# Performance work log

Hardware: AMD Instinct MI355X
Metric: run time of the kernel (lower is better)

Reference implementation:

```python
import jax, jax.numpy as jnp
import numpy as np

B, T, D = 2, 2048, 512
HEADS, DIM_HEAD, MAX_LAG = 8, 64, 5
INNER = HEADS * DIM_HEAD


def setup_inputs() -> dict:
    key = jax.random.key(0)
    k0, k1, k2, k3, k4 = jax.random.split(key, 5)
    x = jax.random.normal(k0, (B, T, D), dtype=jnp.float32)
    # Linear weights stored as (in, out); torch applies x @ W.T with W (out, in).
    Wq = jax.random.normal(k1, (D, INNER), dtype=jnp.float32) * (1.0 / np.sqrt(D))
    Wk = jax.random.normal(k2, (D, INNER), dtype=jnp.float32) * (1.0 / np.sqrt(D))
    Wv = jax.random.normal(k3, (D, INNER), dtype=jnp.float32) * (1.0 / np.sqrt(D))
    Wo = jax.random.normal(k4, (INNER, D), dtype=jnp.float32) * (1.0 / np.sqrt(INNER))
    bo = jnp.zeros((D,), dtype=jnp.float32)
    # Module's init: lag_weights = log(exp(-lags/(max_lag/3))) = -lags/(max_lag/3)
    lags = jnp.arange(MAX_LAG + 1, dtype=jnp.float32)
    lag_weights = jnp.broadcast_to(-(lags / (MAX_LAG / 3.0)), (HEADS, MAX_LAG + 1)).astype(jnp.float32)
    return {"x": x, "Wq": Wq, "Wk": Wk, "Wv": Wv, "Wo": Wo, "bo": bo, "lag_weights": lag_weights}


def reference(x, Wq, Wk, Wv, Wo, bo, lag_weights):
    b, t, _ = x.shape
    h, dh = HEADS, DIM_HEAD
    scale = dh ** -0.5
    # context defaults to x (self-attention)
    q = (x @ Wq).reshape(b, t, h, dh).transpose(0, 2, 1, 3)  # b h t d
    k = (x @ Wk).reshape(b, t, h, dh).transpose(0, 2, 1, 3)
    v = (x @ Wv).reshape(b, t, h, dh).transpose(0, 2, 1, 3)
    sim = jnp.einsum('bhid,bhjd->bhij', q, k) * scale  # b h t t
    # causal mask: keep j <= i
    causal = jnp.tril(jnp.ones((t, t), dtype=bool))
    neg = -jnp.finfo(sim.dtype).max
    sim = jnp.where(causal[None, None], sim, neg)
    # learned additive time-lag bias: lag_adj[h,i,j] = softmax(lag_weights)[h, clamp(i-j,0,MAX_LAG)]
    ti = jnp.arange(t)
    time_lags = jnp.clip(ti[:, None] - ti[None, :], 0, MAX_LAG)  # t t
    lag_probs = jax.nn.softmax(lag_weights, axis=-1)  # h (L+1)
    lag_adj = lag_probs[:, time_lags]  # h t t
    sim = sim + lag_adj[None]
    attn = jax.nn.softmax(sim, axis=-1)
    out = jnp.einsum('bhij,bhjd->bhid', attn, v)
    out = out.transpose(0, 2, 1, 3).reshape(b, t, h * dh)  # b t inner
    return out @ Wo + bo  # dropout is identity at eval
```

## Files before the change

kernel.cpp:

```cpp
#include <hip/hip_runtime.h>
#include <hip/hip_bf16.h>

#define BB 2
#define TT 2048
#define DD 512
#define HH 8
#define DH 64
#define INNER 512
#define MAXLAG 5

typedef __attribute__((ext_vector_type(8))) short short8;
typedef __attribute__((ext_vector_type(4))) float floatx4;
typedef unsigned short ushort_t;

__device__ inline unsigned short f2bf(float f) {
    unsigned u = __float_as_uint(f);
    unsigned r = (u + 0x7FFFu + ((u >> 16) & 1u)) >> 16;
    return (unsigned short)r;
}
__device__ inline float bf2f(unsigned short u) {
    return __uint_as_float(((unsigned)u) << 16);
}

__device__ __forceinline__ void gload16(ushort_t* lds, const ushort_t* g) {
    __builtin_amdgcn_global_load_lds(
        (const __attribute__((address_space(1))) void*)g,
        (__attribute__((address_space(3))) void*)lds, 16, 0, 0);
}

__global__ __launch_bounds__(256)
void cvt_kernel(const float* __restrict__ x,
                const float* __restrict__ wq, const float* __restrict__ wk,
                const float* __restrict__ wv, const float* __restrict__ wo,
                ushort_t* __restrict__ xb,
                ushort_t* __restrict__ wqkvt, ushort_t* __restrict__ wot)
{
    __shared__ float T[32][33];
    const int bid = blockIdx.x;
    if (bid < 1024) {
        int off = (bid * 256 + threadIdx.x) * 8;
        float4 a = *(const float4*)&x[off];
        float4 b = *(const float4*)&x[off + 4];
        ushort_t t[8];
        t[0] = f2bf(a.x); t[1] = f2bf(a.y); t[2] = f2bf(a.z); t[3] = f2bf(a.w);
        t[4] = f2bf(b.x); t[5] = f2bf(b.y); t[6] = f2bf(b.z); t[7] = f2bf(b.w);
        *(uint4*)&xb[off] = *(const uint4*)t;
        return;
    }
    const int r = bid - 1024;
    const int z = r >> 8;
    const int tile = r & 255;
    const float* s = (z == 0) ? wq : (z == 1) ? wk : (z == 2) ? wv : wo;
    ushort_t*    d = (z < 3) ? (wqkvt + (size_t)z * 512 * 512) : wot;
    const int k0 = (tile & 15) * 32;
    const int n0 = (tile >> 4) * 32;
    {
        const int kk = threadIdx.x >> 3;
        const int n4 = (threadIdx.x & 7) * 4;
        float4 v = *(const float4*)&s[(size_t)(k0 + kk) * 512 + n0 + n4];
        T[kk][n4 + 0] = v.x; T[kk][n4 + 1] = v.y;
        T[kk][n4 + 2] = v.z; T[kk][n4 + 3] = v.w;
    }
    __syncthreads();
    {
        const int nn = threadIdx.x >> 3;
        const int k4 = (threadIdx.x & 7) * 4;
        ushort4 o;
        o.x = f2bf(T[k4 + 0][nn]); o.y = f2bf(T[k4 + 1][nn]);
        o.z = f2bf(T[k4 + 2][nn]); o.w = f2bf(T[k4 + 3][nn]);
        *(ushort4*)&d[(size_t)(n0 + nn) * 512 + k0 + k4] = o;
    }
}

#define QM 128
#define QN 64
#define QKS 64

__global__ __launch_bounds__(256)
void gemm_qkv(const ushort_t* __restrict__ A, const ushort_t* __restrict__ Bw,
              ushort_t* __restrict__ q, ushort_t* __restrict__ k,
              ushort_t* __restrict__ vt)
{
    __shared__ ushort_t As[QM * QKS];
    __shared__ ushort_t Bs[QN * QKS];

    const int tid  = threadIdx.x;
    const int wave = tid >> 6;
    const int lane = tid & 63;
    const int quad = lane >> 4;
    const int l15  = lane & 15;
    const int wr   = wave >> 1;
    const int wc   = wave & 1;
    const int bm   = blockIdx.y * QM;
    const int bn   = blockIdx.x * QN;

    const int ga = wave * 256 + lane;
    const ushort_t* ap0 = &A[(size_t)(bm + ((ga +   0) >> 3)) * DD + ((ga +   0) & 7) * 8];
    const ushort_t* ap1 = &A[(size_t)(bm + ((ga +  64) >> 3)) * DD + ((ga +  64) & 7) * 8];
    const ushort_t* ap2 = &A[(size_t)(bm + ((ga + 128) >> 3)) * DD + ((ga + 128) & 7) * 8];
    const ushort_t* ap3 = &A[(size_t)(bm + ((ga + 192) >> 3)) * DD + ((ga + 192) & 7) * 8];
    const int gb = wave * 128 + lane;
    const ushort_t* bp0 = &Bw[(size_t)(bn + ((gb +  0) >> 3)) * DD + ((gb +  0) & 7) * 8];
    const ushort_t* bp1 = &Bw[(size_t)(bn + ((gb + 64) >> 3)) * DD + ((gb + 64) & 7) * 8];
    ushort_t* lA0 = &As[(size_t)(wave * 256 +   0) * 8];
    ushort_t* lA1 = &As[(size_t)(wave * 256 +  64) * 8];
    ushort_t* lA2 = &As[(size_t)(wave * 256 + 128) * 8];
    ushort_t* lA3 = &As[(size_t)(wave * 256 + 192) * 8];
    ushort_t* lB0 = &Bs[(size_t)(wave * 128 +  0) * 8];
    ushort_t* lB1 = &Bs[(size_t)(wave * 128 + 64) * 8];

    floatx4 acc[4][2];
#pragma unroll
    for (int i = 0; i < 4; ++i)
#pragma unroll
        for (int j = 0; j < 2; ++j) acc[i][j] = (floatx4){0.f, 0.f, 0.f, 0.f};

    for (int k0 = 0; k0 < DD; k0 += QKS) {
        __syncthreads();
        gload16(lA0, ap0 + k0);
        gload16(lA1, ap1 + k0);
        gload16(lA2, ap2 + k0);
        gload16(lA3, ap3 + k0);
        gload16(lB0, bp0 + k0);
        gload16(lB1, bp1 + k0);
        __syncthreads();

#pragma unroll
        for (int kk = 0; kk < 2; ++kk) {
            short8 af[4], bfr[2];
#pragma unroll
            for (int mt = 0; mt < 4; ++mt)
                af[mt] = *(const short8*)
                    &As[(((wr * 64 + mt * 16 + l15) << 3) + (kk << 2) + quad) * 8];
#pragma unroll
            for (int nt = 0; nt < 2; ++nt)
                bfr[nt] = *(const short8*)
                    &Bs[(((wc * 32 + nt * 16 + l15) << 3) + (kk << 2) + quad) * 8];
#pragma unroll
            for (int mt = 0; mt < 4; ++mt)
#pragma unroll
                for (int nt = 0; nt < 2; ++nt)
                    acc[mt][nt] = __builtin_amdgcn_mfma_f32_16x16x32_bf16(
                        af[mt], bfr[nt], acc[mt][nt], 0, 0, 0);
        }
    }

    const int z = bn >> 9;
    if (z == 2) {
#pragma unroll
        for (int mt = 0; mt < 4; ++mt) {
            const int m0 = bm + wr * 64 + mt * 16 + quad * 4;
            const int b  = m0 >> 11;
            const int t0 = m0 & 2047;
#pragma unroll
            for (int nt = 0; nt < 2; ++nt) {
                const int n  = bn + wc * 32 + nt * 16 + l15 - 1024;
                const int h  = n >> 6, dd = n & 63;
                ushort4 o;
                o.x = f2bf(acc[mt][nt][0]); o.y = f2bf(acc[mt][nt][1]);
                o.z = f2bf(acc[mt][nt][2]); o.w = f2bf(acc[mt][nt][3]);
                *(ushort4*)&vt[((size_t)((b * 8 + h) * 64 + dd)) * 2048 + t0] = o;
            }
        }
        return;
    }
    ushort_t* O = (z == 0) ? q : k;
    const int nb = bn - z * 512;
#pragma unroll
    for (int mt = 0; mt < 4; ++mt) {
#pragma unroll
        for (int nt = 0; nt < 2; ++nt) {
            const int n = nb + wc * 32 + nt * 16 + l15;
#pragma unroll
            for (int reg = 0; reg < 4; ++reg) {
                const int m = bm + wr * 64 + mt * 16 + quad * 4 + reg;
                O[(size_t)m * 512 + n] = f2bf(acc[mt][nt][reg]);
            }
        }
    }
}

__global__ __launch_bounds__(256)
void gemm_proj(const ushort_t* __restrict__ A, const ushort_t* __restrict__ Bw,
               float* __restrict__ O, const float* __restrict__ bias)
{
    __shared__ ushort_t As[64 * 64];
    __shared__ ushort_t Bs[64 * 64];

    const int tid  = threadIdx.x;
    const int wave = tid >> 6;
    const int lane = tid & 63;
    const int quad = lane >> 4;
    const int l15  = lane & 15;
    const int wr   = wave >> 1;
    const int wc   = wave & 1;
    const int bm   = blockIdx.y * 64;
    const int bn   = blockIdx.x * 64;

    const int g0 = wave * 128 + lane;
    const ushort_t* ap0 = &A[(size_t)(bm + ((g0 +  0) >> 3)) * INNER + ((g0 +  0) & 7) * 8];
    const ushort_t* ap1 = &A[(size_t)(bm + ((g0 + 64) >> 3)) * INNER + ((g0 + 64) & 7) * 8];
    const ushort_t* bp0 = &Bw[(size_t)(bn + ((g0 +  0) >> 3)) * INNER + ((g0 +  0) & 7) * 8];
    const ushort_t* bp1 = &Bw[(size_t)(bn + ((g0 + 64) >> 3)) * INNER + ((g0 + 64) & 7) * 8];
    ushort_t* lA0 = &As[(size_t)(wave * 128 +  0) * 8];
    ushort_t* lA1 = &As[(size_t)(wave * 128 + 64) * 8];
    ushort_t* lB0 = &Bs[(size_t)(wave * 128 +  0) * 8];
    ushort_t* lB1 = &Bs[(size_t)(wave * 128 + 64) * 8];

    floatx4 acc[2][2];
#pragma unroll
    for (int i = 0; i < 2; ++i)
#pragma unroll
        for (int j = 0; j < 2; ++j) acc[i][j] = (floatx4){0.f, 0.f, 0.f, 0.f};

    for (int k0 = 0; k0 < INNER; k0 += 64) {
        __syncthreads();
        gload16(lA0, ap0 + k0);
        gload16(lA1, ap1 + k0);
        gload16(lB0, bp0 + k0);
        gload16(lB1, bp1 + k0);
        __syncthreads();

#pragma unroll
        for (int kk = 0; kk < 2; ++kk) {
            short8 af[2], bfr[2];
#pragma unroll
            for (int mt = 0; mt < 2; ++mt)
                af[mt] = *(const short8*)
                    &As[(((wr * 32 + mt * 16 + l15) << 3) + (kk << 2) + quad) * 8];
#pragma unroll
            for (int nt = 0; nt < 2; ++nt)
                bfr[nt] = *(const short8*)
                    &Bs[(((wc * 32 + nt * 16 + l15) << 3) + (kk << 2) + quad) * 8];
#pragma unroll
            for (int mt = 0; mt < 2; ++mt)
#pragma unroll
                for (int nt = 0; nt < 2; ++nt)
                    acc[mt][nt] = __builtin_amdgcn_mfma_f32_16x16x32_bf16(
                        af[mt], bfr[nt], acc[mt][nt], 0, 0, 0);
        }
    }

    float bv[2];
#pragma unroll
    for (int nt = 0; nt < 2; ++nt)
        bv[nt] = bias[bn + wc * 32 + nt * 16 + l15];
#pragma unroll
    for (int mt = 0; mt < 2; ++mt) {
#pragma unroll
        for (int nt = 0; nt < 2; ++nt) {
            const int n = bn + wc * 32 + nt * 16 + l15;
#pragma unroll
            for (int reg = 0; reg < 4; ++reg) {
                const int m = bm + wr * 32 + mt * 16 + quad * 4 + reg;
                O[(size_t)m * 512 + n] = acc[mt][nt][reg] + bv[nt];
            }
        }
    }
}

#define PAD 72
#define MFIX 10.0f

__global__ __launch_bounds__(256)
void attn_mfma(const ushort_t* __restrict__ Qg,
               const ushort_t* __restrict__ Kg,
               const ushort_t* __restrict__ Vtg,
               const float* __restrict__ lagw,
               ushort_t* __restrict__ ao)
{
    __shared__ ushort_t Ks[64 * 8 * 8];
    __shared__ ushort_t Vts[64 * 8 * 8];
    __shared__ ushort_t Pl[4][16][PAD];

    const int tid  = threadIdx.x;
    const int wave = tid >> 6;
    const int lane = tid & 63;
    const int quad = lane >> 4;
    const int l15  = lane & 15;

    const int f    = blockIdx.x + 32 * blockIdx.y;
    const int half = f >> 8;
    const int r    = f & 255;
    const int bh   = (half << 3) | (r >> 5);
    const int qt   = half ? (r & 31) : (31 - (r & 31));
    const int b    = bh >> 3;
    const int h    = bh & 7;
    const int i0   = qt * 64;
    const int hi   = qt + 1;

    float lagb[MAXLAG + 1];
    {
        float mx = -1e30f;
#pragma unroll
        for (int l = 0; l <= MAXLAG; ++l) {
            lagb[l] = lagw[h * (MAXLAG + 1) + l];
            mx = fmaxf(mx, lagb[l]);
        }
        float s = 0.f;
#pragma unroll
        for (int l = 0; l <= MAXLAG; ++l) { lagb[l] = __expf(lagb[l] - mx); s += lagb[l]; }
        float inv = 1.f / s;
#pragma unroll
        for (int l = 0; l <= MAXLAG; ++l) lagb[l] = lagb[l] * inv - MFIX;
    }
    const float c1  = 0.125f;
    const float c2f = lagb[MAXLAG];

    short8 qf0, qf1;
    {
        const ushort_t* qbase =
            Qg + ((size_t)(b * TT + i0 + wave * 16 + l15)) * INNER + h * DH;
        qf0 = *(const short8*)(qbase + quad * 8);
        qf1 = *(const short8*)(qbase + 32 + quad * 8);
    }

    floatx4 oacc[4];
    float lsum[4] = {0.f, 0.f, 0.f, 0.f};
#pragma unroll
    for (int cb = 0; cb < 4; ++cb) oacc[cb] = (floatx4){0.f, 0.f, 0.f, 0.f};

    const int ibase = i0 + wave * 16 + quad * 4;

    const int srow = tid >> 3;
    const int sc   = tid & 7;
    const ushort_t* Kp0 = Kg + ((size_t)(b * TT) + srow) * INNER + h * DH + sc * 8;
    const ushort_t* Kp1 = Kp0 + (size_t)32 * INNER;
    const ushort_t* Vp0 = Vtg + ((size_t)(bh * 64 + srow)) * 2048 + sc * 8;
    const ushort_t* Vp1 = Vp0 + (size_t)32 * 2048;
    const int slot = (sc + srow) & 7;
    const int kdst0 = ((srow << 3) + slot) << 3;
    const int kdst1 = (((srow + 32) << 3) + slot) << 3;

    uint4 pk0 = *(const uint4*)Kp0;
    uint4 pk1 = *(const uint4*)Kp1;
    uint4 pv0 = *(const uint4*)Vp0;
    uint4 pv1 = *(const uint4*)Vp1;

    for (int kt = 0; kt < hi; ++kt) {
        __syncthreads();
        *(uint4*)&Ks[kdst0]  = pk0;
        *(uint4*)&Ks[kdst1]  = pk1;
        *(uint4*)&Vts[kdst0] = pv0;
        *(uint4*)&Vts[kdst1] = pv1;
        if (kt + 1 < hi) {
            const size_t koff = (size_t)((kt + 1) * 64) * INNER;
            pk0 = *(const uint4*)(Kp0 + koff);
            pk1 = *(const uint4*)(Kp1 + koff);
            pv0 = *(const uint4*)(Vp0 + (kt + 1) * 64);
            pv1 = *(const uint4*)(Vp1 + (kt + 1) * 64);
        }
        __syncthreads();

        const int j0 = kt * 64;

        floatx4 sacc[4];
#pragma unroll
        for (int cb = 0; cb < 4; ++cb) {
            const int key = cb * 16 + l15;
            short8 kf0 = *(const short8*)&Ks[((key << 3) + ((quad + key) & 7)) << 3];
            short8 kf1 = *(const short8*)&Ks[((key << 3) + ((quad + 4 + key) & 7)) << 3];
            floatx4 zf = (floatx4){0.f, 0.f, 0.f, 0.f};
            zf = __builtin_amdgcn_mfma_f32_16x16x32_bf16(qf0, kf0, zf, 0, 0, 0);
            zf = __builtin_amdgcn_mfma_f32_16x16x32_bf16(qf1, kf1, zf, 0, 0, 0);
            sacc[cb] = zf;
        }

        float p[4][4];
        if (i0 + wave * 16 - (j0 + 63) >= MAXLAG) {
#pragma unroll
            for (int cb = 0; cb < 4; ++cb)
#pragma unroll
                for (int reg = 0; reg < 4; ++reg)
                    p[cb][reg] = __expf(fmaf(sacc[cb][reg], c1, c2f));
        } else {
#pragma unroll
            for (int cb = 0; cb < 4; ++cb) {
                const int j = j0 + cb * 16 + l15;
#pragma unroll
                for (int reg = 0; reg < 4; ++reg) {
                    const int lag = (ibase + reg) - j;
                    float bias = (lag <= 0) ? lagb[0]
                               : (lag == 1) ? lagb[1]
                               : (lag == 2) ? lagb[2]
                               : (lag == 3) ? lagb[3]
                               : (lag == 4) ? lagb[4] : lagb[5];
                    float e = __expf(fmaf(sacc[cb][reg], c1, bias));
                    p[cb][reg] = (lag < 0) ? 0.f : e;
                }
            }
        }
#pragma unroll
        for (int cb = 0; cb < 4; ++cb)
#pragma unroll
            for (int reg = 0; reg < 4; ++reg)
                lsum[reg] += p[cb][reg];

#pragma unroll
        for (int cb = 0; cb < 4; ++cb)
#pragma unroll
            for (int reg = 0; reg < 4; ++reg)
                Pl[wave][quad * 4 + reg][cb * 16 + l15] = f2bf(p[cb][reg]);

        short8 pf0 = *(const short8*)&Pl[wave][l15][quad * 8];
        short8 pf1 = *(const short8*)&Pl[wave][l15][32 + quad * 8];

#pragma unroll
        for (int cb = 0; cb < 4; ++cb) {
            const int dd = cb * 16 + l15;
            short8 vf0 = *(const short8*)&Vts[((dd << 3) + ((quad + dd) & 7)) << 3];
            short8 vf1 = *(const short8*)&Vts[((dd << 3) + ((quad + 4 + dd) & 7)) << 3];
            oacc[cb] = __builtin_amdgcn_mfma_f32_16x16x32_bf16(pf0, vf0, oacc[cb], 0, 0, 0);
            oacc[cb] = __builtin_amdgcn_mfma_f32_16x16x32_bf16(pf1, vf1, oacc[cb], 0, 0, 0);
        }
    }

#pragma unroll
    for (int reg = 0; reg < 4; ++reg) {
        lsum[reg] += __shfl_xor(lsum[reg], 1);
        lsum[reg] += __shfl_xor(lsum[reg], 2);
        lsum[reg] += __shfl_xor(lsum[reg], 4);
        lsum[reg] += __shfl_xor(lsum[reg], 8);
    }

#pragma unroll
    for (int reg = 0; reg < 4; ++reg) {
        const int row = ibase + reg;
        const float inv = 1.f / lsum[reg];
        ushort_t* dst = &ao[((size_t)(b * TT + row)) * INNER + h * DH];
#pragma unroll
        for (int cb = 0; cb < 4; ++cb)
            dst[cb * 16 + l15] = f2bf(oacc[cb][reg] * inv);
    }
}

extern "C" void kernel_launch(void* const* d_in, const int* in_sizes, int n_in,
                              void* d_out, int out_size, void* d_ws, size_t ws_size,
                              hipStream_t stream)
{
    const float* x  = (const float*)d_in[0];
    const float* Wq = (const float*)d_in[1];
    const float* Wk = (const float*)d_in[2];
    const float* Wv = (const float*)d_in[3];
    const float* Wo = (const float*)d_in[4];
    const float* bo = (const float*)d_in[5];
    const float* lw = (const float*)d_in[6];
    float* out = (float*)d_out;

    const size_t SZ  = (size_t)BB * TT * INNER;
    const size_t NWE = (size_t)DD * INNER;
    ushort_t* xb    = (ushort_t*)d_ws;
    ushort_t* wqkvt = xb + SZ;
    ushort_t* wot   = wqkvt + 3 * NWE;
    ushort_t* q     = wot + NWE;
    ushort_t* k     = q + SZ;
    ushort_t* vt    = k + SZ;
    ushort_t* ao    = xb;

    cvt_kernel<<<2048, 256, 0, stream>>>(x, Wq, Wk, Wv, Wo, xb, wqkvt, wot);

    dim3 gQKV(3 * INNER / QN, (BB * TT) / QM);
    gemm_qkv<<<gQKV, 256, 0, stream>>>(xb, wqkvt, q, k, vt);

    dim3 gATT(32, BB * HH);
    attn_mfma<<<gATT, 256, 0, stream>>>(q, k, vt, lw, ao);

    dim3 gPRJ(DD / 64, (BB * TT) / 64);
    gemm_proj<<<gPRJ, 256, 0, stream>>>(ao, wot, out, bo);
}
```

Baseline: 130.1 us.

## Double-buffer LDS tiles with swizzled direct loads in GEMM and attention kernels

The QKV GEMM, output projection GEMM and attention kernel now use two LDS buffers. The next K-tile is issued with gload16 into the idle buffer while MFMAs run on the current one, so each iteration needs one barrier instead of two. The GEMM tiles get an XOR-style column swizzle on both the global source offsets and the LDS reads, to cut bank conflicts. The attention kernel drops its register-staged prefetch for direct global-to-LDS loads and wraps its MFMA blocks in s_setprio. The cost is doubled LDS footprint, which may lower occupancy.

```diff
diff --git a/kernel.cpp b/kernel.cpp
--- a/kernel.cpp
+++ b/kernel.cpp
@@ -81,8 +81,8 @@
               ushort_t* __restrict__ q, ushort_t* __restrict__ k,
               ushort_t* __restrict__ vt)
 {
-    __shared__ ushort_t As[QM * QKS];
-    __shared__ ushort_t Bs[QN * QKS];
+    __shared__ ushort_t As[2][QM * QKS];
+    __shared__ ushort_t Bs[2][QN * QKS];
 
     const int tid  = threadIdx.x;
     const int wave = tid >> 6;
@@ -94,20 +94,32 @@
     const int bm   = blockIdx.y * QM;
     const int bn   = blockIdx.x * QN;
 
-    const int ga = wave * 256 + lane;
-    const ushort_t* ap0 = &A[(size_t)(bm + ((ga +   0) >> 3)) * DD + ((ga +   0) & 7) * 8];
-    const ushort_t* ap1 = &A[(size_t)(bm + ((ga +  64) >> 3)) * DD + ((ga +  64) & 7) * 8];
-    const ushort_t* ap2 = &A[(size_t)(bm + ((ga + 128) >> 3)) * DD + ((ga + 128) & 7) * 8];
-    const ushort_t* ap3 = &A[(size_t)(bm + ((ga + 192) >> 3)) * DD + ((ga + 192) & 7) * 8];
-    const int gb = wave * 128 + lane;
-    const ushort_t* bp0 = &Bw[(size_t)(bn + ((gb +  0) >> 3)) * DD + ((gb +  0) & 7) * 8];
-    const ushort_t* bp1 = &Bw[(size_t)(bn + ((gb + 64) >> 3)) * DD + ((gb + 64) & 7) * 8];
-    ushort_t* lA0 = &As[(size_t)(wave * 256 +   0) * 8];
-    ushort_t* lA1 = &As[(size_t)(wave * 256 +  64) * 8];
-    ushort_t* lA2 = &As[(size_t)(wave * 256 + 128) * 8];
-    ushort_t* lA3 = &As[(size_t)(wave * 256 + 192) * 8];
-    ushort_t* lB0 = &Bs[(size_t)(wave * 128 +  0) * 8];
-    ushort_t* lB1 = &Bs[(size_t)(wave * 128 + 64) * 8];
+    const int lr = lane >> 3;
+    const int lc = lane & 7;
+
+    const ushort_t* ap[4];
+#pragma unroll
+    for (int j = 0; j < 4; ++j) {
+        const int row = wave * 32 + j * 8 + lr;
+        const int c   = (lc - row) & 7;
+        ap[j] = &A[(size_t)(bm + row) * DD + c * 8];
+    }
+    const ushort_t* bp[2];
+#pragma unroll
+    for (int j = 0; j < 2; ++j) {
+        const int row = wave * 16 + j * 8 + lr;
+        const int c   = (lc - row) & 7;
+        bp[j] = &Bw[(size_t)(bn + row) * DD + c * 8];
+    }
+
+    auto stage = [&](int buf, int koff) {
+#pragma unroll
+        for (int j = 0; j < 4; ++j)
+            gload16(&As[buf][(wave * 256 + j * 64) * 8], ap[j] + koff);
+#pragma unroll
+        for (int j = 0; j < 2; ++j)
+            gload16(&Bs[buf][(wave * 128 + j * 64) * 8], bp[j] + koff);
+    };
 
     floatx4 acc[4][2];
 #pragma unroll
@@ -115,27 +127,28 @@
 #pragma unroll
         for (int j = 0; j < 2; ++j) acc[i][j] = (floatx4){0.f, 0.f, 0.f, 0.f};
 
+    stage(0, 0);
+    __syncthreads();
+    int cur = 0;
     for (int k0 = 0; k0 < DD; k0 += QKS) {
-        __syncthreads();
-        gload16(lA0, ap0 + k0);
-        gload16(lA1, ap1 + k0);
-        gload16(lA2, ap2 + k0);
-        gload16(lA3, ap3 + k0);
-        gload16(lB0, bp0 + k0);
-        gload16(lB1, bp1 + k0);
-        __syncthreads();
+        const int nxt = k0 + QKS;
+        if (nxt < DD) stage(cur ^ 1, nxt);
 
 #pragma unroll
         for (int kk = 0; kk < 2; ++kk) {
             short8 af[4], bfr[2];
 #pragma unroll
-            for (int mt = 0; mt < 4; ++mt)
+            for (int mt = 0; mt < 4; ++mt) {
+                const int row = wr * 64 + mt * 16 + l15;
                 af[mt] = *(const short8*)
-                    &As[(((wr * 64 + mt * 16 + l15) << 3) + (kk << 2) + quad) * 8];
-#pragma unroll
-            for (int nt = 0; nt < 2; ++nt)
+                    &As[cur][((row << 3) + ((kk * 4 + quad + row) & 7)) * 8];
+            }
+#pragma unroll
+            for (int nt = 0; nt < 2; ++nt) {
+                const int row = wc * 32 + nt * 16 + l15;
                 bfr[nt] = *(const short8*)
-                    &Bs[(((wc * 32 + nt * 16 + l15) << 3) + (kk << 2) + quad) * 8];
+                    &Bs[cur][((row << 3) + ((kk * 4 + quad + row) & 7)) * 8];
+            }
 #pragma unroll
             for (int mt = 0; mt < 4; ++mt)
 #pragma unroll
@@ -143,6 +156,8 @@
                     acc[mt][nt] = __builtin_amdgcn_mfma_f32_16x16x32_bf16(
                         af[mt], bfr[nt], acc[mt][nt], 0, 0, 0);
         }
+        if (nxt < DD) __syncthreads();
+        cur ^= 1;
     }
 
     const int z = bn >> 9;
@@ -184,8 +199,8 @@
 void gemm_proj(const ushort_t* __restrict__ A, const ushort_t* __restrict__ Bw,
                float* __restrict__ O, const float* __restrict__ bias)
 {
-    __shared__ ushort_t As[64 * 64];
-    __shared__ ushort_t Bs[64 * 64];
+    __shared__ ushort_t As[2][64 * 64];
+    __shared__ ushort_t Bs[2][64 * 64];
 
     const int tid  = threadIdx.x;
     const int wave = tid >> 6;
@@ -197,15 +212,26 @@
     const int bm   = blockIdx.y * 64;
     const int bn   = blockIdx.x * 64;
 
-    const int g0 = wave * 128 + lane;
-    const ushort_t* ap0 = &A[(size_t)(bm + ((g0 +  0) >> 3)) * INNER + ((g0 +  0) & 7) * 8];
-    const ushort_t* ap1 = &A[(size_t)(bm + ((g0 + 64) >> 3)) * INNER + ((g0 + 64) & 7) * 8];
-    const ushort_t* bp0 = &Bw[(size_t)(bn + ((g0 +  0) >> 3)) * INNER + ((g0 +  0) & 7) * 8];
-    const ushort_t* bp1 = &Bw[(size_t)(bn + ((g0 + 64) >> 3)) * INNER + ((g0 + 64) & 7) * 8];
-    ushort_t* lA0 = &As[(size_t)(wave * 128 +  0) * 8];
-    ushort_t* lA1 = &As[(size_t)(wave * 128 + 64) * 8];
-    ushort_t* lB0 = &Bs[(size_t)(wave * 128 +  0) * 8];
-    ushort_t* lB1 = &Bs[(size_t)(wave * 128 + 64) * 8];
+    const int lr = lane >> 3;
+    const int lc = lane & 7;
+
+    const ushort_t* ap[2];
+    const ushort_t* bp[2];
+#pragma unroll
+    for (int j = 0; j < 2; ++j) {
+        const int row = wave * 16 + j * 8 + lr;
+        const int c   = (lc - row) & 7;
+        ap[j] = &A[(size_t)(bm + row) * INNER + c * 8];
+        bp[j] = &Bw[(size_t)(bn + row) * INNER + c * 8];
+    }
+
+    auto stage = [&](int buf, int koff) {
+#pragma unroll
+        for (int j = 0; j < 2; ++j) {
+            gload16(&As[buf][(wave * 128 + j * 64) * 8], ap[j] + koff);
+            gload16(&Bs[buf][(wave * 128 + j * 64) * 8], bp[j] + koff);
+        }
+    };
 
     floatx4 acc[2][2];
 #pragma unroll
@@ -213,25 +239,28 @@
 #pragma unroll
         for (int j = 0; j < 2; ++j) acc[i][j] = (floatx4){0.f, 0.f, 0.f, 0.f};
 
+    stage(0, 0);
+    __syncthreads();
+    int cur = 0;
     for (int k0 = 0; k0 < INNER; k0 += 64) {
-        __syncthreads();
-        gload16(lA0, ap0 + k0);
-        gload16(lA1, ap1 + k0);
-        gload16(lB0, bp0 + k0);
-        gload16(lB1, bp1 + k0);
-        __syncthreads();
+        const int nxt = k0 + 64;
+        if (nxt < INNER) stage(cur ^ 1, nxt);
 
 #pragma unroll
         for (int kk = 0; kk < 2; ++kk) {
             short8 af[2], bfr[2];
 #pragma unroll
-            for (int mt = 0; mt < 2; ++mt)
+            for (int mt = 0; mt < 2; ++mt) {
+                const int row = wr * 32 + mt * 16 + l15;
                 af[mt] = *(const short8*)
-                    &As[(((wr * 32 + mt * 16 + l15) << 3) + (kk << 2) + quad) * 8];
-#pragma unroll
-            for (int nt = 0; nt < 2; ++nt)
+                    &As[cur][((row << 3) + ((kk * 4 + quad + row) & 7)) * 8];
+            }
+#pragma unroll
+            for (int nt = 0; nt < 2; ++nt) {
+                const int row = wc * 32 + nt * 16 + l15;
                 bfr[nt] = *(const short8*)
-                    &Bs[(((wc * 32 + nt * 16 + l15) << 3) + (kk << 2) + quad) * 8];
+                    &Bs[cur][((row << 3) + ((kk * 4 + quad + row) & 7)) * 8];
+            }
 #pragma unroll
             for (int mt = 0; mt < 2; ++mt)
 #pragma unroll
@@ -239,6 +268,8 @@
                     acc[mt][nt] = __builtin_amdgcn_mfma_f32_16x16x32_bf16(
                         af[mt], bfr[nt], acc[mt][nt], 0, 0, 0);
         }
+        if (nxt < INNER) __syncthreads();
+        cur ^= 1;
     }
 
     float bv[2];
@@ -269,8 +300,8 @@
                const float* __restrict__ lagw,
                ushort_t* __restrict__ ao)
 {
-    __shared__ ushort_t Ks[64 * 8 * 8];
-    __shared__ ushort_t Vts[64 * 8 * 8];
+    __shared__ ushort_t Ks[2][64 * 8 * 8];
+    __shared__ ushort_t Vts[2][64 * 8 * 8];
     __shared__ ushort_t Pl[4][16][PAD];
 
     const int tid  = threadIdx.x;
@@ -322,49 +353,50 @@
 
     const int ibase = i0 + wave * 16 + quad * 4;
 
-    const int srow = tid >> 3;
-    const int sc   = tid & 7;
-    const ushort_t* Kp0 = Kg + ((size_t)(b * TT) + srow) * INNER + h * DH + sc * 8;
-    const ushort_t* Kp1 = Kp0 + (size_t)32 * INNER;
-    const ushort_t* Vp0 = Vtg + ((size_t)(bh * 64 + srow)) * 2048 + sc * 8;
-    const ushort_t* Vp1 = Vp0 + (size_t)32 * 2048;
-    const int slot = (sc + srow) & 7;
-    const int kdst0 = ((srow << 3) + slot) << 3;
-    const int kdst1 = (((srow + 32) << 3) + slot) << 3;
-
-    uint4 pk0 = *(const uint4*)Kp0;
-    uint4 pk1 = *(const uint4*)Kp1;
-    uint4 pv0 = *(const uint4*)Vp0;
-    uint4 pv1 = *(const uint4*)Vp1;
+    const int lr = lane >> 3;
+    const int lc = lane & 7;
+    const ushort_t* ksrc[2];
+    const ushort_t* vsrc[2];
+#pragma unroll
+    for (int j = 0; j < 2; ++j) {
+        const int row = wave * 16 + j * 8 + lr;
+        const int c   = (lc - row) & 7;
+        ksrc[j] = Kg + ((size_t)(b * TT) + row) * INNER + h * DH + c * 8;
+        vsrc[j] = Vtg + ((size_t)(bh * 64 + row)) * 2048 + c * 8;
+    }
+
+    auto stage = [&](int buf, int kt) {
+        const size_t ko = (size_t)kt * 64 * INNER;
+        const int    vo = kt * 64;
+#pragma unroll
+        for (int j = 0; j < 2; ++j) {
+            gload16(&Ks[buf][(wave * 128 + j * 64) * 8],  ksrc[j] + ko);
+            gload16(&Vts[buf][(wave * 128 + j * 64) * 8], vsrc[j] + vo);
+        }
+    };
+
+    stage(0, 0);
+    __syncthreads();
+    int cur = 0;
 
     for (int kt = 0; kt < hi; ++kt) {
-        __syncthreads();
-        *(uint4*)&Ks[kdst0]  = pk0;
-        *(uint4*)&Ks[kdst1]  = pk1;
-        *(uint4*)&Vts[kdst0] = pv0;
-        *(uint4*)&Vts[kdst1] = pv1;
-        if (kt + 1 < hi) {
-            const size_t koff = (size_t)((kt + 1) * 64) * INNER;
-            pk0 = *(const uint4*)(Kp0 + koff);
-            pk1 = *(const uint4*)(Kp1 + koff);
-            pv0 = *(const uint4*)(Vp0 + (kt + 1) * 64);
-            pv1 = *(const uint4*)(Vp1 + (kt + 1) * 64);
-        }
-        __syncthreads();
+        if (kt + 1 < hi) stage(cur ^ 1, kt + 1);
 
         const int j0 = kt * 64;
 
         floatx4 sacc[4];
+        __builtin_amdgcn_s_setprio(1);
 #pragma unroll
         for (int cb = 0; cb < 4; ++cb) {
             const int key = cb * 16 + l15;
-            short8 kf0 = *(const short8*)&Ks[((key << 3) + ((quad + key) & 7)) << 3];
-            short8 kf1 = *(const short8*)&Ks[((key << 3) + ((quad + 4 + key) & 7)) << 3];
+            short8 kf0 = *(const short8*)&Ks[cur][((key << 3) + ((quad + key) & 7)) << 3];
+            short8 kf1 = *(const short8*)&Ks[cur][((key << 3) + ((quad + 4 + key) & 7)) << 3];
             floatx4 zf = (floatx4){0.f, 0.f, 0.f, 0.f};
             zf = __builtin_amdgcn_mfma_f32_16x16x32_bf16(qf0, kf0, zf, 0, 0, 0);
             zf = __builtin_amdgcn_mfma_f32_16x16x32_bf16(qf1, kf1, zf, 0, 0, 0);
             sacc[cb] = zf;
         }
+        __builtin_amdgcn_s_setprio(0);
 
         float p[4][4];
         if (i0 + wave * 16 - (j0 + 63) >= MAXLAG) {
@@ -405,14 +437,19 @@
         short8 pf0 = *(const short8*)&Pl[wave][l15][quad * 8];
         short8 pf1 = *(const short8*)&Pl[wave][l15][32 + quad * 8];
 
+        __builtin_amdgcn_s_setprio(1);
 #pragma unroll
         for (int cb = 0; cb < 4; ++cb) {
             const int dd = cb * 16 + l15;
-            short8 vf0 = *(const short8*)&Vts[((dd << 3) + ((quad + dd) & 7)) << 3];
-            short8 vf1 = *(const short8*)&Vts[((dd << 3) + ((quad + 4 + dd) & 7)) << 3];
+            short8 vf0 = *(const short8*)&Vts[cur][((dd << 3) + ((quad + dd) & 7)) << 3];
+            short8 vf1 = *(const short8*)&Vts[cur][((dd << 3) + ((quad + 4 + dd) & 7)) << 3];
             oacc[cb] = __builtin_amdgcn_mfma_f32_16x16x32_bf16(pf0, vf0, oacc[cb], 0, 0, 0);
             oacc[cb] = __builtin_amdgcn_mfma_f32_16x16x32_bf16(pf1, vf1, oacc[cb], 0, 0, 0);
         }
+        __builtin_amdgcn_s_setprio(0);
+
+        if (kt + 1 < hi) __syncthreads();
+        cur ^= 1;
     }
 
 #pragma unroll
```

Measured after the change: 137.0 us. +5.3%, slower.

## Split attention key range into chunks and add a combine kernel

Applied to the files above, without the earlier changes.

Each query tile's causal key range is split into chunks of up to 8 key tiles, processed by separate blocks (1280 total). Each block writes an unnormalized bf16 partial output and a row sum. A new combine kernel sums the partials and normalizes. This shortens the per-block critical path and improves CU load balance, at the cost of an extra launch, extra global traffic, and bf16 rounding of the partials.

```diff
diff --git a/kernel.cpp b/kernel.cpp
--- a/kernel.cpp
+++ b/kernel.cpp
@@ -267,7 +267,8 @@
                const ushort_t* __restrict__ Kg,
                const ushort_t* __restrict__ Vtg,
                const float* __restrict__ lagw,
-               ushort_t* __restrict__ ao)
+               ushort_t* __restrict__ Opart,
+               float* __restrict__ Lpart)
 {
     __shared__ ushort_t Ks[64 * 8 * 8];
     __shared__ ushort_t Vts[64 * 8 * 8];
@@ -279,15 +280,20 @@
     const int quad = lane >> 4;
     const int l15  = lane & 15;
 
-    const int f    = blockIdx.x + 32 * blockIdx.y;
-    const int half = f >> 8;
-    const int r    = f & 255;
-    const int bh   = (half << 3) | (r >> 5);
-    const int qt   = half ? (r & 31) : (31 - (r & 31));
-    const int b    = bh >> 3;
-    const int h    = bh & 7;
-    const int i0   = qt * 64;
-    const int hi   = qt + 1;
+    const int f  = blockIdx.x;
+    const int rr = f >> 4;
+    const int bh = f & 15;
+    int qt, ci;
+    if (rr < 32)      { qt = 31 - (rr >> 2); ci = rr & 3; }
+    else if (rr < 56) { const int t = rr - 32; qt = 23 - t / 3; ci = t % 3; }
+    else if (rr < 72) { const int t = rr - 56; qt = 15 - (t >> 1); ci = t & 1; }
+    else              { qt = 79 - rr; ci = 0; }
+    const int lo = ci * 8;
+    const int hi = min(lo + 8, qt + 1);
+
+    const int b  = bh >> 3;
+    const int h  = bh & 7;
+    const int i0 = qt * 64;
 
     float lagb[MAXLAG + 1];
     {
@@ -332,12 +338,16 @@
     const int kdst0 = ((srow << 3) + slot) << 3;
     const int kdst1 = (((srow + 32) << 3) + slot) << 3;
 
-    uint4 pk0 = *(const uint4*)Kp0;
-    uint4 pk1 = *(const uint4*)Kp1;
-    uint4 pv0 = *(const uint4*)Vp0;
-    uint4 pv1 = *(const uint4*)Vp1;
-
-    for (int kt = 0; kt < hi; ++kt) {
+    uint4 pk0, pk1, pv0, pv1;
+    {
+        const size_t koff = (size_t)(lo * 64) * INNER;
+        pk0 = *(const uint4*)(Kp0 + koff);
+        pk1 = *(const uint4*)(Kp1 + koff);
+        pv0 = *(const uint4*)(Vp0 + lo * 64);
+        pv1 = *(const uint4*)(Vp1 + lo * 64);
+    }
+
+    for (int kt = lo; kt < hi; ++kt) {
         __syncthreads();
         *(uint4*)&Ks[kdst0]  = pk0;
         *(uint4*)&Ks[kdst1]  = pk1;
@@ -426,12 +436,45 @@
 #pragma unroll
     for (int reg = 0; reg < 4; ++reg) {
         const int row = ibase + reg;
-        const float inv = 1.f / lsum[reg];
-        ushort_t* dst = &ao[((size_t)(b * TT + row)) * INNER + h * DH];
+        const size_t obase = ((size_t)(ci * 16 + bh) * TT + row) * 64;
 #pragma unroll
         for (int cb = 0; cb < 4; ++cb)
-            dst[cb * 16 + l15] = f2bf(oacc[cb][reg] * inv);
-    }
+            Opart[obase + cb * 16 + l15] = f2bf(oacc[cb][reg]);
+        if (l15 == 0)
+            Lpart[(size_t)(ci * 16 + bh) * TT + row] = lsum[reg];
+    }
+}
+
+#define CMB_UNITS (16 * TT * 16)
+
+__global__ __launch_bounds__(256)
+void combine_kernel(const ushort_t* __restrict__ Opart,
+                    const float* __restrict__ Lpart,
+                    ushort_t* __restrict__ ao)
+{
+    int u = blockIdx.x * 256 + threadIdx.x;
+    const int bh  = u >> 15;
+    const int rem = u & 32767;
+    const int i   = rem >> 4;
+    const int d   = (rem & 15) * 4;
+    const int b   = bh >> 3;
+    const int h   = bh & 7;
+    const int nch = ((i >> 6) >> 3) + 1;
+
+    float s0 = 0.f, s1 = 0.f, s2 = 0.f, s3 = 0.f, l = 0.f;
+    for (int ci = 0; ci < nch; ++ci) {
+        const size_t p = ((size_t)(ci * 16 + bh) * TT + i) * 64 + d;
+        ushort4 a = *(const ushort4*)&Opart[p];
+        s0 += bf2f(a.x); s1 += bf2f(a.y); s2 += bf2f(a.z); s3 += bf2f(a.w);
+        l  += Lpart[(size_t)(ci * 16 + bh) * TT + i];
+    }
+    const float inv = 1.f / l;
+    ushort4 o;
+    o.x = f2bf(s0 * inv);
+    o.y = f2bf(s1 * inv);
+    o.z = f2bf(s2 * inv);
+    o.w = f2bf(s3 * inv);
+    *(ushort4*)&ao[((size_t)(b * TT + i)) * INNER + h * DH + d] = o;
 }
 
 extern "C" void kernel_launch(void* const* d_in, const int* in_sizes, int n_in,
@@ -455,6 +498,8 @@
     ushort_t* q     = wot + NWE;
     ushort_t* k     = q + SZ;
     ushort_t* vt    = k + SZ;
+    ushort_t* opart = vt + SZ;
+    float*    lpart = (float*)(opart + 4 * (size_t)16 * TT * 64);
     ushort_t* ao    = xb;
 
     cvt_kernel<<<2048, 256, 0, stream>>>(x, Wq, Wk, Wv, Wo, xb, wqkvt, wot);
@@ -462,8 +507,9 @@
     dim3 gQKV(3 * INNER / QN, (BB * TT) / QM);
     gemm_qkv<<<gQKV, 256, 0, stream>>>(xb, wqkvt, q, k, vt);
 
-    dim3 gATT(32, BB * HH);
-    attn_mfma<<<gATT, 256, 0, stream>>>(q, k, vt, lw, ao);
+    attn_mfma<<<1280, 256, 0, stream>>>(q, k, vt, lw, opart, lpart);
+
+    combine_kernel<<<CMB_UNITS / 256, 256, 0, stream>>>(opart, lpart, ao);
 
     dim3 gPRJ(DD / 64, (BB * TT) / 64);
     gemm_proj<<<gPRJ, 256, 0, stream>>>(ao, wot, out, bo);
```

Result: no change. 128.9 us (-0.9%).
